# Performance work log

Hardware: AMD Instinct MI355X
Metric: run time of the kernel (lower is better)

The kernel has to match this reference:

```python
import jax, jax.numpy as jnp
import numpy as np

B, IN, H, L, OUT, T, S0 = 512, 64, 512, 2, 12, 31, 8
HEAD = (T - 1) / 2  # 15.0
EPS = 1e-5


def setup_inputs() -> dict:
    key = jax.random.key(0)
    ks = jax.random.split(key, 10)
    s = 0.05
    return {
        "Wih0": jax.random.normal(ks[0], (4 * H, IN), jnp.float32) * s,
        "Whh0": jax.random.normal(ks[1], (4 * H, H), jnp.float32) * s,
        "b0": jax.random.normal(ks[2], (4 * H,), jnp.float32) * s,
        "Wih1": jax.random.normal(ks[3], (4 * H, H), jnp.float32) * s,
        "Whh1": jax.random.normal(ks[4], (4 * H, H), jnp.float32) * s,
        "b1": jax.random.normal(ks[5], (4 * H,), jnp.float32) * s,
        "gamma": jnp.ones((H,), jnp.float32),
        "beta": jnp.zeros((H,), jnp.float32),
        "Wout": jax.random.normal(ks[6], (OUT, H), jnp.float32) * s,
        "bout": jax.random.normal(ks[7], (OUT,), jnp.float32) * s,
        "h0": jax.random.uniform(ks[8], (L, H), jnp.float32),
        "c0": jax.random.uniform(ks[9], (L, H), jnp.float32),
    }


def _lstm_layer(xs, h0, c0, Wih, Whh, b):
    # xs: (B, d_in) treated as an unbatched sequence of length B (torch semantics here).
    def step(carry, x):
        h, c = carry
        g = x @ Wih.T + h @ Whh.T + b  # (4H,)
        i, f, gg, o = jnp.split(g, 4, axis=-1)  # torch gate order: i, f, g, o
        c = jax.nn.sigmoid(f) * c + jax.nn.sigmoid(i) * jnp.tanh(gg)
        h = jax.nn.sigmoid(o) * jnp.tanh(c)
        return (h, c), h
    (hT, cT), ys = jax.lax.scan(step, (h0, c0), xs)
    return ys, hT, cT


def reference(Wih0, Whh0, b0, Wih1, Whh1, b1, gamma, beta, Wout, bout, h0, c0):
    keys = jax.random.split(jax.random.key(42), T)
    x = jnp.ones((B, IN), jnp.float32)
    h, c = h0, c0  # (L, H)
    acts, lps = [], []
    for i in range(T):
        ys0, h0n, c0n = _lstm_layer(x, h[0], c[0], Wih0, Whh0, b0)
        ys1, h1n, c1n = _lstm_layer(ys0, h[1], c[1], Wih1, Whh1, b1)
        h = jnp.stack([h0n, h1n])
        c = jnp.stack([c0n, c1n])
        # BatchNorm1d, training mode (biased variance over the B dim)
        mu = ys1.mean(0)
        var = ys1.var(0)
        yn = (ys1 - mu) / jnp.sqrt(var + EPS) * gamma + beta
        g = jnp.exp(-yn ** 2)  # GaussianActivation
        logits = g @ Wout.T + bout  # (B, OUT)
        if i < HEAD:
            action = jax.random.categorical(keys[i], logits, axis=-1)
        else:
            action = jax.random.categorical(keys[i], logits[:, S0:], axis=-1) + S0
        # log_prob under the FULL categorical (as in the original code)
        lp = jax.nn.log_softmax(logits, axis=-1)[jnp.arange(B), action]
        acts.append(action)
        lps.append(lp)
    return jnp.stack(acts), jnp.stack(lps)  # ((T,B) int, (T,B) float)
```

## Files before the change

kernel.cpp:

```cpp
#include <hip/hip_runtime.h>
#include <stdint.h>
#include <math.h>

#define Bv      512
#define INv     64
#define Hv      512
#define OUTv    12
#define Tv      31
#define S0v     8
#define STEPS   (Tv*Bv)

#define KA      16
#define KB      32
#define KPP     16
#define NBLK    (KA+KB+KPP)
#define RING    32


__device__ __forceinline__ uint32_t rotl32(uint32_t v, int r){ return (v<<r)|(v>>(32-r)); }

__device__ __forceinline__ void threefry2x32(uint32_t k0, uint32_t k1,
                                             uint32_t x0, uint32_t x1,
                                             uint32_t& o0, uint32_t& o1) {
  uint32_t ks2 = k0 ^ k1 ^ 0x1BD11BDAu;
  x0 += k0; x1 += k1;
#define TFR(r) { x0 += x1; x1 = rotl32(x1, r); x1 ^= x0; }
  TFR(13) TFR(15) TFR(26) TFR(6)
  x0 += k1;  x1 += ks2 + 1u;
  TFR(17) TFR(29) TFR(16) TFR(24)
  x0 += ks2; x1 += k0 + 2u;
  TFR(13) TFR(15) TFR(26) TFR(6)
  x0 += k0;  x1 += k1 + 3u;
  TFR(17) TFR(29) TFR(16) TFR(24)
  x0 += k1;  x1 += ks2 + 4u;
  TFR(13) TFR(15) TFR(26) TFR(6)
  x0 += ks2; x1 += k0 + 5u;
#undef TFR
  o0 = x0; o1 = x1;
}

__device__ __forceinline__ uint32_t tf_bits32(uint32_t k0, uint32_t k1, uint32_t j) {
  uint32_t a, b;
  threefry2x32(k0, k1, 0u, j, a, b);
  return a ^ b;
}

__device__ __forceinline__ float u32_to_uniform(uint32_t bits) {
  float f = __uint_as_float(0x3F800000u | (bits >> 9)) - 1.0f;
  const float TINY = 1.17549435e-38f;
  return fmaxf(TINY, f + TINY);
}

__device__ __forceinline__ float gumbelf(uint32_t bits) {
  float u = u32_to_uniform(bits);
  return -logf(-logf(u));
}

__device__ __forceinline__ float sigmf(float x) {
  if (x >= 0.f) { float z = expf(-x); return 1.f/(1.f+z); }
  float z = expf(x); return z/(1.f+z);
}

template<int N>
__device__ __forceinline__ void bfly_halve(float* v, int m) {
  int lane = threadIdx.x & 63;
  bool up = (lane & m) != 0;
#pragma unroll
  for (int j = 0; j < N/2; ++j) {
    float send = up ? v[j] : v[j + N/2];
    float recv = __shfl_xor(send, m, 64);
    v[j] = (up ? v[j + N/2] : v[j]) + recv;
  }
}

__device__ __forceinline__ uint64_t aload64(const uint64_t* p){
  return __hip_atomic_load(p, __ATOMIC_RELAXED, __HIP_MEMORY_SCOPE_AGENT);
}
__device__ __forceinline__ void astore64(uint64_t* p, uint64_t v){
  __hip_atomic_store(p, v, __ATOMIC_RELAXED, __HIP_MEMORY_SCOPE_AGENT);
}
__device__ __forceinline__ uint32_t aload32(const uint32_t* p){
  return __hip_atomic_load(p, __ATOMIC_RELAXED, __HIP_MEMORY_SCOPE_AGENT);
}
__device__ __forceinline__ void astore32(uint32_t* p, uint32_t v){
  __hip_atomic_store(p, v, __ATOMIC_RELAXED, __HIP_MEMORY_SCOPE_AGENT);
}
__device__ __forceinline__ uint32_t tagof(uint64_t w){ return (uint32_t)(w>>32); }
__device__ __forceinline__ float    valof(uint64_t w){ return __uint_as_float((uint32_t)w); }
__device__ __forceinline__ uint64_t mkword(uint32_t t, float v){
  return ((uint64_t)t<<32) | (uint64_t)__float_as_uint(v);
}

__global__ __launch_bounds__(512, 1)
void net_persistent(const float* __restrict__ Wih0, const float* __restrict__ Whh0,
                    const float* __restrict__ b0,
                    const float* __restrict__ Wih1, const float* __restrict__ Whh1,
                    const float* __restrict__ b1,
                    const float* __restrict__ gamma, const float* __restrict__ beta,
                    const float* __restrict__ Wout, const float* __restrict__ bout,
                    const float* __restrict__ h0in, const float* __restrict__ c0in,
                    float* __restrict__ out, uint32_t* __restrict__ wsu)
{
  uint32_t* iterflag = wsu;
  uint64_t* h0A = (uint64_t*)((char*)wsu + 4096);
  uint64_t* h0B = (uint64_t*)((char*)wsu + 4096 + (size_t)RING*Hv*8);
  uint64_t* y1c = (uint64_t*)((char*)wsu + 4096 + (size_t)2*RING*Hv*8);
  float*    ys1 = (float*)((char*)wsu + 4096 + (size_t)3*RING*Hv*8);

  const int bid  = blockIdx.x;
  const int tid  = threadIdx.x;
  const int wave = tid >> 6;
  const int lane = tid & 63;

  __shared__ float hbuf[2][Hv];
  __shared__ float xbuf[2][2*Hv];
  __shared__ float Wout_s[OUTv*Hv];
  __shared__ float mu_s[Hv], isd_s[Hv], gam_s[Hv], bet_s[Hv];

  if (bid < KA) {
    const int hbase = bid*32;
    float w[128];
#pragma unroll
    for (int jl = 0; jl < 4; ++jl)
#pragma unroll
      for (int g = 0; g < 4; ++g) {
        int r = jl*4 + g;
        const float* rp = Whh0 + (size_t)(g*Hv + hbase + wave*4 + jl)*Hv;
#pragma unroll
        for (int k = 0; k < 2; ++k) {
          float4 q = *(const float4*)(rp + k*256 + lane*4);
          w[r*8+k*4+0]=q.x; w[r*8+k*4+1]=q.y; w[r*8+k*4+2]=q.z; w[r*8+k*4+3]=q.w;
        }
      }
    const int jsel = lane & 3;
    const int hg = hbase + wave*4 + jsel;
    float cgi, cgf, cgg, cgo;
    {
      float s0=b0[0*Hv+hg], s1=b0[1*Hv+hg], s2=b0[2*Hv+hg], s3=b0[3*Hv+hg];
      for (int k = 0; k < INv; ++k) {
        s0 += Wih0[(size_t)(0*Hv+hg)*INv+k];
        s1 += Wih0[(size_t)(1*Hv+hg)*INv+k];
        s2 += Wih0[(size_t)(2*Hv+hg)*INv+k];
        s3 += Wih0[(size_t)(3*Hv+hg)*INv+k];
      }
      cgi=s0; cgf=s1; cgg=s2; cgo=s3;
    }
    float cst = c0in[hg];

    for (int s = 0; s < STEPS; ++s) {
      const int par = s & 1;
      if ((s & 15) == 0 && s >= 32) {
        const uint64_t* tp = y1c + (size_t)((s-17)&(RING-1))*Hv + lane*8;
        uint32_t need = (uint32_t)(s - 16);
        for (;;) {
          uint32_t t = tagof(aload64(tp));
          if (__all((int)(t >= need && t <= (uint32_t)STEPS))) break;
          __builtin_amdgcn_s_sleep(1);
        }
      }
      {
        int idx = tid;
        if (s == 0) {
          hbuf[0][idx] = h0in[idx];
        } else {
          const uint64_t* src = h0A + (size_t)((s-1)&(RING-1))*Hv + idx;
          uint32_t want = (uint32_t)s;
          uint64_t a = aload64(src);
          while (tagof(a) != want) a = aload64(src);
          hbuf[par][idx] = valof(a);
        }
      }
      __syncthreads();
      const float4* hv = (const float4*)(hbuf[par]);
      float4 vA = hv[lane], vB = hv[64 + lane];
      float acc[16];
#pragma unroll
      for (int r = 0; r < 16; ++r) {
        float a = 0.f;
        a = fmaf(w[r*8+0], vA.x, a); a = fmaf(w[r*8+1], vA.y, a);
        a = fmaf(w[r*8+2], vA.z, a); a = fmaf(w[r*8+3], vA.w, a);
        a = fmaf(w[r*8+4], vB.x, a); a = fmaf(w[r*8+5], vB.y, a);
        a = fmaf(w[r*8+6], vB.z, a); a = fmaf(w[r*8+7], vB.w, a);
        acc[r] = a;
      }
      bfly_halve<16>(acc, 32);
      bfly_halve<8>(acc, 16);
      bfly_halve<4>(acc, 8);
      bfly_halve<2>(acc, 4);
      acc[0] += __shfl_xor(acc[0], 2, 64);
      acc[0] += __shfl_xor(acc[0], 1, 64);
      float gi = __shfl(acc[0], 16*jsel + 0,  64);
      float gf = __shfl(acc[0], 16*jsel + 4,  64);
      float gg = __shfl(acc[0], 16*jsel + 8,  64);
      float go = __shfl(acc[0], 16*jsel + 12, 64);
      float cc = sigmf(gf+cgf)*cst + sigmf(gi+cgi)*tanhf(gg+cgg);
      float hh = sigmf(go+cgo)*tanhf(cc);
      cst = cc;
      if (lane < 8) {
        uint64_t* dst = (lane < 4) ? h0A : h0B;
        astore64(dst + (size_t)(s&(RING-1))*Hv + hg, mkword((uint32_t)(s+1), hh));
      }
    }
  } else if (bid < KA + KB) {
    const int wg1 = bid - KA;
    const int hbase = wg1*16;
    float w[128];
#pragma unroll
    for (int jl = 0; jl < 2; ++jl)
#pragma unroll
      for (int g = 0; g < 4; ++g) {
        int r = jl*4 + g;
        int row = g*Hv + hbase + wave*2 + jl;
#pragma unroll
        for (int k = 0; k < 4; ++k) {
          int col = k*256 + lane*4;
          const float* M = (col < Hv) ? (Wih1 + (size_t)row*Hv + col)
                                      : (Whh1 + (size_t)row*Hv + (col - Hv));
          float4 q = *(const float4*)M;
          w[r*16+k*4+0]=q.x; w[r*16+k*4+1]=q.y; w[r*16+k*4+2]=q.z; w[r*16+k*4+3]=q.w;
        }
      }
    const int jsel = lane & 1;
    const int hg = hbase + wave*2 + jsel;
    float cgi = b1[0*Hv+hg], cgf = b1[1*Hv+hg],
          cgg = b1[2*Hv+hg], cgo = b1[3*Hv+hg];
    float cst = c0in[Hv + hg];

    for (int s = 0; s < STEPS; ++s) {
      const int par = s & 1;
      {
        int j0 = tid*2;
        if (j0 < Hv) {
          const uint64_t* src = h0B + (size_t)(s&(RING-1))*Hv + j0;
          uint32_t want = (uint32_t)(s+1);
          uint64_t a = aload64(src), b2 = aload64(src+1);
          while (tagof(a) != want || tagof(b2) != want) {
            a = aload64(src); b2 = aload64(src+1);
          }
          xbuf[par][j0] = valof(a); xbuf[par][j0+1] = valof(b2);
        } else {
          if (s == 0) {
            xbuf[0][j0]   = h0in[j0];
            xbuf[0][j0+1] = h0in[j0+1];
          } else {
            const uint64_t* src = y1c + (size_t)((s-1)&(RING-1))*Hv + (j0 - Hv);
            uint32_t want = (uint32_t)s;
            uint64_t a = aload64(src), b2 = aload64(src+1);
            while (tagof(a) != want || tagof(b2) != want) {
              a = aload64(src); b2 = aload64(src+1);
            }
            xbuf[par][j0] = valof(a); xbuf[par][j0+1] = valof(b2);
          }
        }
      }
      __syncthreads();
      const float4* xv = (const float4*)(xbuf[par]);
      float4 v0 = xv[lane], v1 = xv[64+lane], v2 = xv[128+lane], v3 = xv[192+lane];
      float acc[8];
#pragma unroll
      for (int r = 0; r < 8; ++r) {
        float a = 0.f;
        a = fmaf(w[r*16+ 0], v0.x, a); a = fmaf(w[r*16+ 1], v0.y, a);
        a = fmaf(w[r*16+ 2], v0.z, a); a = fmaf(w[r*16+ 3], v0.w, a);
        a = fmaf(w[r*16+ 4], v1.x, a); a = fmaf(w[r*16+ 5], v1.y, a);
        a = fmaf(w[r*16+ 6], v1.z, a); a = fmaf(w[r*16+ 7], v1.w, a);
        a = fmaf(w[r*16+ 8], v2.x, a); a = fmaf(w[r*16+ 9], v2.y, a);
        a = fmaf(w[r*16+10], v2.z, a); a = fmaf(w[r*16+11], v2.w, a);
        a = fmaf(w[r*16+12], v3.x, a); a = fmaf(w[r*16+13], v3.y, a);
        a = fmaf(w[r*16+14], v3.z, a); a = fmaf(w[r*16+15], v3.w, a);
        acc[r] = a;
      }
      bfly_halve<8>(acc, 32);
      bfly_halve<4>(acc, 16);
      bfly_halve<2>(acc, 8);
      acc[0] += __shfl_xor(acc[0], 4, 64);
      acc[0] += __shfl_xor(acc[0], 2, 64);
      acc[0] += __shfl_xor(acc[0], 1, 64);
      float gi = __shfl(acc[0], 32*jsel + 0,  64);
      float gf = __shfl(acc[0], 32*jsel + 8,  64);
      float gg = __shfl(acc[0], 32*jsel + 16, 64);
      float go = __shfl(acc[0], 32*jsel + 24, 64);
      float cc = sigmf(gf+cgf)*cst + sigmf(gi+cgi)*tanhf(gg+cgg);
      float hh = sigmf(go+cgo)*tanhf(cc);
      cst = cc;
      if (lane < 2) {
        astore64(y1c + (size_t)(s&(RING-1))*Hv + hg, mkword((uint32_t)(s+1), hh));
        ys1[(size_t)s*Hv + hg] = hh;
      }
      if ((s & 511) == 511) {
        __syncthreads();
        if (tid == 0) {
          __builtin_amdgcn_fence(__ATOMIC_RELEASE, "agent");
          astore32(iterflag + wg1, (uint32_t)((s >> 9) + 1));
        }
      }
    }
  } else {
    const int p = bid - KA - KB;
    for (int r = tid; r < OUTv*Hv; r += 512) Wout_s[r] = Wout[r];
    for (int h = tid; h < Hv; h += 512) { gam_s[h] = gamma[h]; bet_s[h] = beta[h]; }
    float bo[OUTv];
#pragma unroll
    for (int o = 0; o < OUTv; ++o) bo[o] = bout[o];
    __syncthreads();

    for (int i = p; i < Tv; i += KPP) {
      const uint32_t tgt = (uint32_t)(i + 1);
      if (tid < 64) {
        for (;;) {
          uint32_t v = aload32(iterflag + (lane & 31));
          if (__all((int)(v >= tgt && v <= (uint32_t)Tv))) break;
          __builtin_amdgcn_s_sleep(16);
        }
      }
      __syncthreads();
      __builtin_amdgcn_fence(__ATOMIC_ACQUIRE, "agent");

      const float* Y = ys1 + (size_t)i * Bv * Hv;

      for (int h = tid; h < Hv; h += 512) {
        double sum = 0.0, sq = 0.0;
        for (int b = 0; b < Bv; ++b) {
          double v = (double)Y[(size_t)b*Hv + h];
          sum += v; sq += v*v;
        }
        double mu = sum * (1.0/512.0);
        double var = sq * (1.0/512.0) - mu*mu;
        if (var < 0.0) var = 0.0;
        mu_s[h]  = (float)mu;
        isd_s[h] = (float)(1.0 / sqrt(var + 1e-5));
      }
      __syncthreads();

      uint32_t k0, k1;
      threefry2x32(0u, 42u, 0u, (uint32_t)i, k0, k1);

      for (int b = tid; b < Bv; b += 512) {
        float lg[OUTv];
#pragma unroll
        for (int o = 0; o < OUTv; ++o) lg[o] = 0.f;
        const float* Yb = Y + (size_t)b * Hv;
        for (int h = 0; h < Hv; ++h) {
          float yn = (Yb[h] - mu_s[h]) * isd_s[h] * gam_s[h] + bet_s[h];
          float gv = expf(-yn*yn);
#pragma unroll
          for (int o = 0; o < OUTv; ++o) lg[o] = fmaf(gv, Wout_s[o*Hv + h], lg[o]);
        }
#pragma unroll
        for (int o = 0; o < OUTv; ++o) lg[o] += bo[o];

        int action; float la;
        if (i < 15) {
          float best = -3.0e38f; int bi = 0; float bl = lg[0];
#pragma unroll
          for (int o = 0; o < OUTv; ++o) {
            uint32_t bits = tf_bits32(k0, k1, (uint32_t)(b*12 + o));
            float z = gumbelf(bits) + lg[o];
            if (z > best) { best = z; bi = o; bl = lg[o]; }
          }
          action = bi; la = bl;
        } else {
          float best = -3.0e38f; int bi = 0; float bl = lg[S0v];
#pragma unroll
          for (int o = 0; o < 4; ++o) {
            uint32_t bits = tf_bits32(k0, k1, (uint32_t)(b*4 + o));
            float z = gumbelf(bits) + lg[S0v + o];
            if (z > best) { best = z; bi = o; bl = lg[S0v + o]; }
          }
          action = S0v + bi; la = bl;
        }

        float mx = lg[0];
#pragma unroll
        for (int o = 1; o < OUTv; ++o) mx = fmaxf(mx, lg[o]);
        float se = 0.f;
#pragma unroll
        for (int o = 0; o < OUTv; ++o) se += expf(lg[o] - mx);
        float lp = (la - mx) - logf(se);

        out[i*Bv + b]         = (float)action;
        out[STEPS + i*Bv + b] = lp;
      }
    }
  }
}

extern "C" void kernel_launch(void* const* d_in, const int* in_sizes, int n_in,
                              void* d_out, int out_size, void* d_ws, size_t ws_size,
                              hipStream_t stream) {
  const float* Wih0 = (const float*)d_in[0];
  const float* Whh0 = (const float*)d_in[1];
  const float* b0   = (const float*)d_in[2];
  const float* Wih1 = (const float*)d_in[3];
  const float* Whh1 = (const float*)d_in[4];
  const float* b1   = (const float*)d_in[5];
  const float* gam  = (const float*)d_in[6];
  const float* bet  = (const float*)d_in[7];
  const float* Wout = (const float*)d_in[8];
  const float* bout = (const float*)d_in[9];
  const float* h0   = (const float*)d_in[10];
  const float* c0   = (const float*)d_in[11];

  net_persistent<<<dim3(NBLK), dim3(512), 0, stream>>>(
      Wih0, Whh0, b0, Wih1, Whh1, b1, gam, bet, Wout, bout, h0, c0,
      (float*)d_out, (uint32_t*)d_ws);
}
```

Measured before the change: 41.36 ms.

## Spread role blocks across XCDs and add plain-store/sc0-load fast path for handoff

Launches 256 blocks and assigns roles by bid&7, so layer-0, layer-1 and post-processing groups each sit on a single XCD (assuming round-robin block dispatch across XCDs). Same-XCD consumers then poll via plain stores and sc0 loads that should hit the shared L2, with a fallback to agent-scope atomic words after repeated misses. The ring shrinks to 16 and the layer-0 throttle check moves to every 8 steps. This adds idle blocks and relies on undocumented placement and coherence behaviour, which could cause stalls or a silent fallback to the slow path.

```diff
diff --git a/kernel.cpp b/kernel.cpp
--- a/kernel.cpp
+++ b/kernel.cpp
@@ -13,8 +13,8 @@
 #define KA      16
 #define KB      32
 #define KPP     16
-#define NBLK    (KA+KB+KPP)
-#define RING    32
+#define NBLK    256
+#define RING    16
 
 
 __device__ __forceinline__ uint32_t rotl32(uint32_t v, int r){ return (v<<r)|(v>>(32-r)); }
@@ -85,6 +85,15 @@
 __device__ __forceinline__ void astore32(uint32_t* p, uint32_t v){
   __hip_atomic_store(p, v, __ATOMIC_RELAXED, __HIP_MEMORY_SCOPE_AGENT);
 }
+__device__ __forceinline__ void store_plain64(uint64_t* p, uint64_t v){
+  asm volatile("global_store_dwordx2 %0, %1, off" :: "v"(p), "v"(v) : "memory");
+}
+__device__ __forceinline__ uint64_t load_sc0(const uint64_t* p){
+  uint64_t r;
+  asm volatile("global_load_dwordx2 %0, %1, off sc0\n\ts_waitcnt vmcnt(0)"
+               : "=&v"(r) : "v"(p) : "memory");
+  return r;
+}
 __device__ __forceinline__ uint32_t tagof(uint64_t w){ return (uint32_t)(w>>32); }
 __device__ __forceinline__ float    valof(uint64_t w){ return __uint_as_float((uint32_t)w); }
 __device__ __forceinline__ uint64_t mkword(uint32_t t, float v){
@@ -105,20 +114,23 @@
   uint64_t* h0A = (uint64_t*)((char*)wsu + 4096);
   uint64_t* h0B = (uint64_t*)((char*)wsu + 4096 + (size_t)RING*Hv*8);
   uint64_t* y1c = (uint64_t*)((char*)wsu + 4096 + (size_t)2*RING*Hv*8);
-  float*    ys1 = (float*)((char*)wsu + 4096 + (size_t)3*RING*Hv*8);
+  uint64_t* yL  = (uint64_t*)((char*)wsu + 4096 + (size_t)3*RING*Hv*8);
+  float*    ys1 = (float*)((char*)wsu + 4096 + (size_t)4*RING*Hv*8);
 
   const int bid  = blockIdx.x;
   const int tid  = threadIdx.x;
   const int wave = tid >> 6;
   const int lane = tid & 63;
+  const int role = bid & 7;
+  const int sub  = bid >> 3;
 
   __shared__ float hbuf[2][Hv];
   __shared__ float xbuf[2][2*Hv];
   __shared__ float Wout_s[OUTv*Hv];
   __shared__ float mu_s[Hv], isd_s[Hv], gam_s[Hv], bet_s[Hv];
 
-  if (bid < KA) {
-    const int hbase = bid*32;
+  if (role == 0 && sub < KA) {
+    const int hbase = sub*32;
     float w[128];
 #pragma unroll
     for (int jl = 0; jl < 4; ++jl)
@@ -146,12 +158,14 @@
       cgi=s0; cgf=s1; cgg=s2; cgo=s3;
     }
     float cst = c0in[hg];
+    bool fbL = false;
+    int  fbAcc = 0;
 
     for (int s = 0; s < STEPS; ++s) {
       const int par = s & 1;
-      if ((s & 15) == 0 && s >= 32) {
-        const uint64_t* tp = y1c + (size_t)((s-17)&(RING-1))*Hv + lane*8;
-        uint32_t need = (uint32_t)(s - 16);
+      if ((s & 7) == 0 && s >= 16) {
+        const uint64_t* tp = y1c + (size_t)((s-9)&(RING-1))*Hv + lane*8;
+        uint32_t need = (uint32_t)(s - 8);
         for (;;) {
           uint32_t t = tagof(aload64(tp));
           if (__all((int)(t >= need && t <= (uint32_t)STEPS))) break;
@@ -163,10 +177,23 @@
         if (s == 0) {
           hbuf[0][idx] = h0in[idx];
         } else {
-          const uint64_t* src = h0A + (size_t)((s-1)&(RING-1))*Hv + idx;
+          const int slot = (s-1)&(RING-1);
+          uint64_t* lp = h0A + (size_t)slot*Hv + idx;
+          const uint64_t* ap = h0B + (size_t)slot*Hv + idx;
           uint32_t want = (uint32_t)s;
-          uint64_t a = aload64(src);
-          while (tagof(a) != want) a = aload64(src);
+          uint64_t a = 0; bool got = false;
+          if (!fbL) {
+            int it = 0;
+            for (;;) {
+              a = load_sc0(lp);
+              if (tagof(a) == want) { got = true; break; }
+              if (++it > 4) { if (++fbAcc > 8192) { fbL = true; break; } }
+            }
+          }
+          if (!got) {
+            a = aload64(ap);
+            while (tagof(a) != want) a = aload64(ap);
+          }
           hbuf[par][idx] = valof(a);
         }
       }
@@ -197,12 +224,14 @@
       float hh = sigmf(go+cgo)*tanhf(cc);
       cst = cc;
       if (lane < 8) {
-        uint64_t* dst = (lane < 4) ? h0A : h0B;
-        astore64(dst + (size_t)(s&(RING-1))*Hv + hg, mkword((uint32_t)(s+1), hh));
+        uint64_t w64 = mkword((uint32_t)(s+1), hh);
+        size_t off = (size_t)(s&(RING-1))*Hv + hg;
+        if (lane < 4) store_plain64(h0A + off, w64);
+        else          astore64(h0B + off, w64);
       }
     }
-  } else if (bid < KA + KB) {
-    const int wg1 = bid - KA;
+  } else if (role == 1) {
+    const int wg1 = sub;
     const int hbase = wg1*16;
     float w[128];
 #pragma unroll
@@ -225,6 +254,8 @@
     float cgi = b1[0*Hv+hg], cgf = b1[1*Hv+hg],
           cgg = b1[2*Hv+hg], cgo = b1[3*Hv+hg];
     float cst = c0in[Hv + hg];
+    bool fbL = false;
+    int  fbAcc = 0;
 
     for (int s = 0; s < STEPS; ++s) {
       const int par = s & 1;
@@ -243,11 +274,24 @@
             xbuf[0][j0]   = h0in[j0];
             xbuf[0][j0+1] = h0in[j0+1];
           } else {
-            const uint64_t* src = y1c + (size_t)((s-1)&(RING-1))*Hv + (j0 - Hv);
+            const int slot = (s-1)&(RING-1);
+            uint64_t* lp = yL + (size_t)slot*Hv + (j0 - Hv);
+            const uint64_t* ap = y1c + (size_t)slot*Hv + (j0 - Hv);
             uint32_t want = (uint32_t)s;
-            uint64_t a = aload64(src), b2 = aload64(src+1);
-            while (tagof(a) != want || tagof(b2) != want) {
-              a = aload64(src); b2 = aload64(src+1);
+            uint64_t a = 0, b2 = 0; bool got = false;
+            if (!fbL) {
+              int it = 0;
+              for (;;) {
+                a = load_sc0(lp); b2 = load_sc0(lp+1);
+                if (tagof(a) == want && tagof(b2) == want) { got = true; break; }
+                if (++it > 4) { if (++fbAcc > 8192) { fbL = true; break; } }
+              }
+            }
+            if (!got) {
+              a = aload64(ap); b2 = aload64(ap+1);
+              while (tagof(a) != want || tagof(b2) != want) {
+                a = aload64(ap); b2 = aload64(ap+1);
+              }
             }
             xbuf[par][j0] = valof(a); xbuf[par][j0+1] = valof(b2);
           }
@@ -283,9 +327,12 @@
       float cc = sigmf(gf+cgf)*cst + sigmf(gi+cgi)*tanhf(gg+cgg);
       float hh = sigmf(go+cgo)*tanhf(cc);
       cst = cc;
-      if (lane < 2) {
-        astore64(y1c + (size_t)(s&(RING-1))*Hv + hg, mkword((uint32_t)(s+1), hh));
-        ys1[(size_t)s*Hv + hg] = hh;
+      {
+        uint64_t w64 = mkword((uint32_t)(s+1), hh);
+        size_t off = (size_t)(s&(RING-1))*Hv + hg;
+        if (lane < 2)      store_plain64(yL + off, w64);
+        else if (lane < 4) astore64(y1c + off, w64);
+        else if (lane < 6) ys1[(size_t)s*Hv + hg] = hh;
       }
       if ((s & 511) == 511) {
         __syncthreads();
@@ -295,8 +342,8 @@
         }
       }
     }
-  } else {
-    const int p = bid - KA - KB;
+  } else if (role == 2 && sub < KPP) {
+    const int p = sub;
     for (int r = tid; r < OUTv*Hv; r += 512) Wout_s[r] = Wout[r];
     for (int h = tid; h < Hv; h += 512) { gam_s[h] = gamma[h]; bet_s[h] = beta[h]; }
     float bo[OUTv];
```

Result: slower. 126.7 ms (+206.2%).

## Poll tagged ring directly into registers per wave, drop LDS staging and barrier

Applied to the files above, without the earlier changes.

Each wave now spin-loads the tagged h/y words it needs straight from global memory into registers, replacing the cooperative block-wide copy into shared memory and the per-step __syncthreads. The aim is to take the block barrier off the critical path of the recurrent dependency chain. The publishing stores also become atomic exchanges, presumably so they reach the coherent cache sooner. The cost is that every wave issues redundant atomic loads (8 or 16 per lane per step) and keeps polling, which raises memory traffic.

```diff
diff --git a/kernel.cpp b/kernel.cpp
--- a/kernel.cpp
+++ b/kernel.cpp
@@ -76,8 +76,8 @@
 __device__ __forceinline__ uint64_t aload64(const uint64_t* p){
   return __hip_atomic_load(p, __ATOMIC_RELAXED, __HIP_MEMORY_SCOPE_AGENT);
 }
-__device__ __forceinline__ void astore64(uint64_t* p, uint64_t v){
-  __hip_atomic_store(p, v, __ATOMIC_RELAXED, __HIP_MEMORY_SCOPE_AGENT);
+__device__ __forceinline__ void aswap64(uint64_t* p, uint64_t v){
+  (void)__hip_atomic_exchange(p, v, __ATOMIC_RELAXED, __HIP_MEMORY_SCOPE_AGENT);
 }
 __device__ __forceinline__ uint32_t aload32(const uint32_t* p){
   return __hip_atomic_load(p, __ATOMIC_RELAXED, __HIP_MEMORY_SCOPE_AGENT);
@@ -112,8 +112,6 @@
   const int wave = tid >> 6;
   const int lane = tid & 63;
 
-  __shared__ float hbuf[2][Hv];
-  __shared__ float xbuf[2][2*Hv];
   __shared__ float Wout_s[OUTv*Hv];
   __shared__ float mu_s[Hv], isd_s[Hv], gam_s[Hv], bet_s[Hv];
 
@@ -146,9 +144,9 @@
       cgi=s0; cgf=s1; cgg=s2; cgo=s3;
     }
     float cst = c0in[hg];
+    const int c0 = 4*lane, c1 = 256 + 4*lane;
 
     for (int s = 0; s < STEPS; ++s) {
-      const int par = s & 1;
       if ((s & 15) == 0 && s >= 32) {
         const uint64_t* tp = y1c + (size_t)((s-17)&(RING-1))*Hv + lane*8;
         uint32_t need = (uint32_t)(s - 16);
@@ -158,21 +156,26 @@
           __builtin_amdgcn_s_sleep(1);
         }
       }
-      {
-        int idx = tid;
-        if (s == 0) {
-          hbuf[0][idx] = h0in[idx];
-        } else {
-          const uint64_t* src = h0A + (size_t)((s-1)&(RING-1))*Hv + idx;
-          uint32_t want = (uint32_t)s;
-          uint64_t a = aload64(src);
-          while (tagof(a) != want) a = aload64(src);
-          hbuf[par][idx] = valof(a);
-        }
-      }
-      __syncthreads();
-      const float4* hv = (const float4*)(hbuf[par]);
-      float4 vA = hv[lane], vB = hv[64 + lane];
+      float4 vA, vB;
+      if (s == 0) {
+        vA = *(const float4*)(h0in + c0);
+        vB = *(const float4*)(h0in + c1);
+      } else {
+        const uint64_t* base = h0A + (size_t)((s-1)&(RING-1))*Hv;
+        const uint32_t want = (uint32_t)s;
+        uint64_t a0,a1,a2,a3,b0w,b1w,b2w,b3w;
+        for (;;) {
+          a0 = aload64(base+c0+0); a1 = aload64(base+c0+1);
+          a2 = aload64(base+c0+2); a3 = aload64(base+c0+3);
+          b0w= aload64(base+c1+0); b1w= aload64(base+c1+1);
+          b2w= aload64(base+c1+2); b3w= aload64(base+c1+3);
+          if (tagof(a0)==want && tagof(a1)==want && tagof(a2)==want && tagof(a3)==want &&
+              tagof(b0w)==want && tagof(b1w)==want && tagof(b2w)==want && tagof(b3w)==want)
+            break;
+        }
+        vA.x=valof(a0); vA.y=valof(a1); vA.z=valof(a2); vA.w=valof(a3);
+        vB.x=valof(b0w); vB.y=valof(b1w); vB.z=valof(b2w); vB.w=valof(b3w);
+      }
       float acc[16];
 #pragma unroll
       for (int r = 0; r < 16; ++r) {
@@ -198,7 +201,7 @@
       cst = cc;
       if (lane < 8) {
         uint64_t* dst = (lane < 4) ? h0A : h0B;
-        astore64(dst + (size_t)(s&(RING-1))*Hv + hg, mkword((uint32_t)(s+1), hh));
+        aswap64(dst + (size_t)(s&(RING-1))*Hv + hg, mkword((uint32_t)(s+1), hh));
       }
     }
   } else if (bid < KA + KB) {
@@ -225,37 +228,47 @@
     float cgi = b1[0*Hv+hg], cgf = b1[1*Hv+hg],
           cgg = b1[2*Hv+hg], cgo = b1[3*Hv+hg];
     float cst = c0in[Hv + hg];
+    const int c0 = 4*lane, c1 = 256 + 4*lane;
 
     for (int s = 0; s < STEPS; ++s) {
-      const int par = s & 1;
+      float4 v0, v1, v2, v3;
       {
-        int j0 = tid*2;
-        if (j0 < Hv) {
-          const uint64_t* src = h0B + (size_t)(s&(RING-1))*Hv + j0;
-          uint32_t want = (uint32_t)(s+1);
-          uint64_t a = aload64(src), b2 = aload64(src+1);
-          while (tagof(a) != want || tagof(b2) != want) {
-            a = aload64(src); b2 = aload64(src+1);
+        const uint64_t* bx = h0B + (size_t)(s&(RING-1))*Hv;
+        const uint32_t wantx = (uint32_t)(s+1);
+        if (s == 0) {
+          v2 = *(const float4*)(h0in + 512 + c0);
+          v3 = *(const float4*)(h0in + 512 + c1);
+          uint64_t x0,x1,x2,x3,x4,x5,x6,x7;
+          for (;;) {
+            x0=aload64(bx+c0+0); x1=aload64(bx+c0+1); x2=aload64(bx+c0+2); x3=aload64(bx+c0+3);
+            x4=aload64(bx+c1+0); x5=aload64(bx+c1+1); x6=aload64(bx+c1+2); x7=aload64(bx+c1+3);
+            if (tagof(x0)==wantx && tagof(x1)==wantx && tagof(x2)==wantx && tagof(x3)==wantx &&
+                tagof(x4)==wantx && tagof(x5)==wantx && tagof(x6)==wantx && tagof(x7)==wantx)
+              break;
           }
-          xbuf[par][j0] = valof(a); xbuf[par][j0+1] = valof(b2);
+          v0.x=valof(x0); v0.y=valof(x1); v0.z=valof(x2); v0.w=valof(x3);
+          v1.x=valof(x4); v1.y=valof(x5); v1.z=valof(x6); v1.w=valof(x7);
         } else {
-          if (s == 0) {
-            xbuf[0][j0]   = h0in[j0];
-            xbuf[0][j0+1] = h0in[j0+1];
-          } else {
-            const uint64_t* src = y1c + (size_t)((s-1)&(RING-1))*Hv + (j0 - Hv);
-            uint32_t want = (uint32_t)s;
-            uint64_t a = aload64(src), b2 = aload64(src+1);
-            while (tagof(a) != want || tagof(b2) != want) {
-              a = aload64(src); b2 = aload64(src+1);
-            }
-            xbuf[par][j0] = valof(a); xbuf[par][j0+1] = valof(b2);
+          const uint64_t* by = y1c + (size_t)((s-1)&(RING-1))*Hv;
+          const uint32_t wanty = (uint32_t)s;
+          uint64_t x0,x1,x2,x3,x4,x5,x6,x7, y0,y1,y2,y3,y4,y5,y6,y7;
+          for (;;) {
+            x0=aload64(bx+c0+0); x1=aload64(bx+c0+1); x2=aload64(bx+c0+2); x3=aload64(bx+c0+3);
+            x4=aload64(bx+c1+0); x5=aload64(bx+c1+1); x6=aload64(bx+c1+2); x7=aload64(bx+c1+3);
+            y0=aload64(by+c0+0); y1=aload64(by+c0+1); y2=aload64(by+c0+2); y3=aload64(by+c0+3);
+            y4=aload64(by+c1+0); y5=aload64(by+c1+1); y6=aload64(by+c1+2); y7=aload64(by+c1+3);
+            if (tagof(x0)==wantx && tagof(x1)==wantx && tagof(x2)==wantx && tagof(x3)==wantx &&
+                tagof(x4)==wantx && tagof(x5)==wantx && tagof(x6)==wantx && tagof(x7)==wantx &&
+                tagof(y0)==wanty && tagof(y1)==wanty && tagof(y2)==wanty && tagof(y3)==wanty &&
+                tagof(y4)==wanty && tagof(y5)==wanty && tagof(y6)==wanty && tagof(y7)==wanty)
+              break;
           }
-        }
-      }
-      __syncthreads();
-      const float4* xv = (const float4*)(xbuf[par]);
-      float4 v0 = xv[lane], v1 = xv[64+lane], v2 = xv[128+lane], v3 = xv[192+lane];
+          v0.x=valof(x0); v0.y=valof(x1); v0.z=valof(x2); v0.w=valof(x3);
+          v1.x=valof(x4); v1.y=valof(x5); v1.z=valof(x6); v1.w=valof(x7);
+          v2.x=valof(y0); v2.y=valof(y1); v2.z=valof(y2); v2.w=valof(y3);
+          v3.x=valof(y4); v3.y=valof(y5); v3.z=valof(y6); v3.w=valof(y7);
+        }
+      }
       float acc[8];
 #pragma unroll
       for (int r = 0; r < 8; ++r) {
@@ -284,7 +297,7 @@
       float hh = sigmf(go+cgo)*tanhf(cc);
       cst = cc;
       if (lane < 2) {
-        astore64(y1c + (size_t)(s&(RING-1))*Hv + hg, mkword((uint32_t)(s+1), hh));
+        aswap64(y1c + (size_t)(s&(RING-1))*Hv + hg, mkword((uint32_t)(s+1), hh));
         ys1[(size_t)s*Hv + hg] = hh;
       }
       if ((s & 511) == 511) {
```

Result: slower. 110.1 ms (+166.3%).
